# Performance work log

Hardware: AMD Instinct MI355X
Metric: run time of the kernel (lower is better)

The kernel has to match this reference:

```python
import jax, jax.numpy as jnp
import numpy as np

N = 50000   # nodes
E = 800000  # edges (avg degree 16)
C = 128     # hidden_channels
G = 128     # graphs in batch
L0, L1 = 512, 256  # linear_hidden_channels
P = 2       # num_params (output per graph)


def setup_inputs() -> dict:
    key = jax.random.key(0)
    ks = iter(jax.random.split(key, 48))

    def w(shape):
        return jax.random.normal(next(ks), shape, jnp.float32) / np.float32(np.sqrt(shape[0]))

    inp = {}
    inp["x"] = jax.random.normal(next(ks), (N, 4), jnp.float32)
    inp["edge_index"] = jax.random.randint(next(ks), (2, E), 0, N, dtype=jnp.int32)
    inp["edge_attr"] = jax.random.normal(next(ks), (E, 3), jnp.float32)
    inp["batch"] = jnp.sort(jax.random.randint(next(ks), (N,), 0, G, dtype=jnp.int32))
    # TransformerConv params: layer 0 (in=4) and shared layer (in=C, applied twice
    # because `[GConv(...)]*(n-1)` reuses the same module object).
    for i, din in enumerate([4, C]):
        inp[f"Wq{i}"] = w((din, C)); inp[f"bq{i}"] = jnp.zeros((C,), jnp.float32)
        inp[f"Wk{i}"] = w((din, C)); inp[f"bk{i}"] = jnp.zeros((C,), jnp.float32)
        inp[f"Wv{i}"] = w((din, C)); inp[f"bv{i}"] = jnp.zeros((C,), jnp.float32)
        inp[f"We{i}"] = w((3, C))   # lin_edge has no bias
        inp[f"Ws{i}"] = w((din, C)); inp[f"bs{i}"] = jnp.zeros((C,), jnp.float32)
    inp["Wl0"] = w((C, L0));  inp["bl0"] = jnp.zeros((L0,), jnp.float32)
    inp["Wl1"] = w((L0, L1)); inp["bl1"] = jnp.zeros((L1,), jnp.float32)
    inp["Wl2"] = w((L1, P));  inp["bl2"] = jnp.zeros((P,), jnp.float32)
    return inp


def tconv(x, src, dst, e_attr, Wq, bq, Wk, bk, Wv, bv, We, Ws, bs):
    # TransformerConv (heads=1, edge_dim, root_weight=True, beta=False)
    n = x.shape[0]
    c = Wq.shape[1]
    q = x @ Wq + bq            # [N, C]
    k = x @ Wk + bk
    v = x @ Wv + bv
    e = e_attr @ We            # [E, C]
    kj = k[src] + e            # [E, C] key at source + edge emb
    vj = v[src] + e            # [E, C] value at source + edge emb
    logits = jnp.sum(q[dst] * kj, axis=-1) / jnp.sqrt(jnp.float32(c))  # [E]
    # softmax over incoming edges of each target node
    m = jax.ops.segment_max(logits, dst, num_segments=n)
    a = jnp.exp(logits - m[dst])
    denom = jax.ops.segment_sum(a, dst, num_segments=n)
    alpha = a / denom[dst]
    out = jax.ops.segment_sum(vj * alpha[:, None], dst, num_segments=n)
    return out + x @ Ws + bs   # root/skip connection


def reference(x, edge_index, edge_attr, batch,
              Wq0, bq0, Wk0, bk0, Wv0, bv0, We0, Ws0, bs0,
              Wq1, bq1, Wk1, bk1, Wv1, bv1, We1, Ws1, bs1,
              Wl0, bl0, Wl1, bl1, Wl2, bl2):
    src, dst = edge_index[0], edge_index[1]
    # layer 0
    h = tconv(x, src, dst, edge_attr, Wq0, bq0, Wk0, bk0, Wv0, bv0, We0, Ws0, bs0)
    h = jax.nn.leaky_relu(h, 0.01)  # dropout is identity in eval
    # layers 1..2 share weights (Python list-multiplication of modules)
    for _ in range(2):
        h = tconv(h, src, dst, edge_attr, Wq1, bq1, Wk1, bk1, Wv1, bv1, We1, Ws1, bs1)
        h = jax.nn.leaky_relu(h, 0.01)
    # global_add_pool
    g = jax.ops.segment_sum(h, batch, num_segments=G)  # [G, C]
    # MLP head
    g = jax.nn.relu(g @ Wl0 + bl0)
    g = jax.nn.relu(g @ Wl1 + bl1)
    g = g @ Wl2 + bl2                                  # [G, 2]
    return jnp.ravel(g)                                # [G*2]
```

## Files before the change

### kernel.cpp

```cpp
#include <hip/hip_runtime.h>
#include <math.h>

#define N_NODES 50000
#define N_EDGES 800000
#define CDIM    128
#define GDIM    128
#define L0DIM   512
#define L1DIM   256

typedef unsigned int uint;
typedef unsigned short ushort;
typedef __attribute__((ext_vector_type(8))) short short8;
typedef __attribute__((ext_vector_type(4))) float f32x4;

#define QSCALE 0.12751744f

__device__ inline ushort f2bf(float f) {
  uint u = __float_as_uint(f);
  uint r = (u + 0x7fffu + ((u >> 16) & 1u)) >> 16;
  return (ushort)r;
}
__device__ inline float bflo(uint u) { return __uint_as_float(u << 16); }
__device__ inline float bfhi(uint u) { return __uint_as_float(u & 0xffff0000u); }

__global__ void hist_kernel(const int* __restrict__ dst, int* counts, int E) {
  int e = blockIdx.x * 256 + threadIdx.x;
  if (e < E) atomicAdd(&counts[dst[e]], 1);
}

__global__ void scan_blocks(const int* __restrict__ counts, int* excl, int* bsums, int N) {
  __shared__ int s[1024];
  int tid = threadIdx.x;
  int i = blockIdx.x * 1024 + tid;
  int v = (i < N) ? counts[i] : 0;
  s[tid] = v;
  __syncthreads();
  for (int off = 1; off < 1024; off <<= 1) {
    int t = (tid >= off) ? s[tid - off] : 0;
    __syncthreads();
    s[tid] += t;
    __syncthreads();
  }
  if (i < N) excl[i] = s[tid] - v;
  if (tid == 1023) bsums[blockIdx.x] = s[1023];
}

__global__ void scan_sums(int* bsums, int nb) {
  int lane = threadIdx.x;
  int orig = (lane < nb) ? bsums[lane] : 0;
  int v = orig;
#pragma unroll
  for (int off = 1; off < 64; off <<= 1) {
    int t = __shfl_up(v, off);
    if (lane >= off) v += t;
  }
  if (lane < nb) bsums[lane] = v - orig;
}

__global__ void scan_add(const int* __restrict__ excl, const int* __restrict__ bsums,
                         int* indptr, int N, int E) {
  int i = blockIdx.x * 1024 + threadIdx.x;
  if (i < N) indptr[i] = excl[i] + bsums[blockIdx.x];
  if (i == 0) indptr[N] = E;
}

__global__ void scatter2_kernel(const int* __restrict__ dst, const int* __restrict__ src,
                                const float* __restrict__ attr,
                                const int* __restrict__ indptr,
                                int* cursor, int* csr_src, float4* csr_attr, int E) {
  int e = blockIdx.x * 256 + threadIdx.x;
  if (e < E) {
    int d = dst[e];
    int pos = atomicAdd(&cursor[d], 1);
    int i = indptr[d] + pos;
    csr_src[i] = src[e];
    csr_attr[i] = make_float4(attr[e * 3 + 0], attr[e * 3 + 1], attr[e * 3 + 2], 0.f);
  }
}

__global__ void l0_qkvs(const float* __restrict__ x,
                        const float* __restrict__ Wq, const float* __restrict__ bq,
                        const float* __restrict__ Wk, const float* __restrict__ bk,
                        const float* __restrict__ Wv, const float* __restrict__ bv,
                        const float* __restrict__ Ws, const float* __restrict__ bs,
                        ushort* __restrict__ q, ushort* __restrict__ kvb,
                        float* __restrict__ hs, int N) {
  __shared__ float W[4][4][128];
  __shared__ float B[4][128];
  int tid = threadIdx.x;
  for (int i = tid; i < 4 * 128; i += 256) {
    W[0][i >> 7][i & 127] = Wq[i];
    W[1][i >> 7][i & 127] = Wk[i];
    W[2][i >> 7][i & 127] = Wv[i];
    W[3][i >> 7][i & 127] = Ws[i];
  }
  for (int i = tid; i < 128; i += 256) {
    B[0][i] = bq[i]; B[1][i] = bk[i]; B[2][i] = bv[i]; B[3][i] = bs[i];
  }
  __syncthreads();
  int gid = blockIdx.x * 256 + tid;
  int n = gid >> 7, c = gid & 127;
  if (n >= N) return;
  float x0 = x[n * 4 + 0], x1 = x[n * 4 + 1], x2 = x[n * 4 + 2], x3 = x[n * 4 + 3];
  float qv = x0 * W[0][0][c] + x1 * W[0][1][c] + x2 * W[0][2][c] + x3 * W[0][3][c] + B[0][c];
  float kv = x0 * W[1][0][c] + x1 * W[1][1][c] + x2 * W[1][2][c] + x3 * W[1][3][c] + B[1][c];
  float vv = x0 * W[2][0][c] + x1 * W[2][1][c] + x2 * W[2][2][c] + x3 * W[2][3][c] + B[2][c];
  float sv = x0 * W[3][0][c] + x1 * W[3][1][c] + x2 * W[3][2][c] + x3 * W[3][3][c] + B[3][c];
  q[(size_t)n * 128 + c] = f2bf(qv * QSCALE);
  kvb[(size_t)n * 256 + c]       = f2bf(kv);
  kvb[(size_t)n * 256 + 128 + c] = f2bf(vv);
  hs[n * 128 + c] = sv;
}

__global__ void prep_w(const float* __restrict__ Wq, const float* __restrict__ Wk,
                       const float* __restrict__ Wv, const float* __restrict__ Ws,
                       ushort* __restrict__ wt) {
  int idx = blockIdx.x * 256 + threadIdx.x;
  int z = idx >> 14, rem = idx & 16383;
  int k_ = rem >> 7, c_ = rem & 127;
  const float* W = (z == 0) ? Wq : (z == 1) ? Wk : (z == 2) ? Wv : Ws;
  wt[z * 16384 + c_ * 128 + k_] = f2bf(W[k_ * 128 + c_]);
}

#define LDA 136
__global__ __launch_bounds__(256) void gemm_mfma(
    const float* __restrict__ H, const ushort* __restrict__ wtg,
    const float* __restrict__ bq, const float* __restrict__ bk,
    const float* __restrict__ bv, const float* __restrict__ bs,
    ushort* __restrict__ q, ushort* __restrict__ kvb,
    float* __restrict__ hs, int N) {
  __shared__ ushort Alds[64 * LDA];
  __shared__ ushort Wlds[128 * LDA];
  int tid = threadIdx.x;
  int n0 = blockIdx.x * 64;

  {
    uint* al = (uint*)Alds;
    for (int i = tid; i < 4096; i += 256) {
      int r = i >> 6, kp = i & 63;
      int grow = n0 + r; grow = (grow < N) ? grow : (N - 1);
      float2 hv = *(const float2*)&H[(size_t)grow * 128 + 2 * kp];
      al[r * (LDA / 2) + kp] = (uint)f2bf(hv.x) | ((uint)f2bf(hv.y) << 16);
    }
  }

  int w = tid >> 6, lane = tid & 63;
  int m_ = lane & 15, quad = lane >> 4;

  for (int z = 0; z < 4; z++) {
    __syncthreads();
    {
      const uint* wg = (const uint*)(wtg + z * 16384);
      uint* wl = (uint*)Wlds;
      for (int i = tid; i < 8192; i += 256) {
        int c_ = i >> 6, kp = i & 63;
        wl[c_ * (LDA / 2) + kp] = wg[c_ * 64 + kp];
      }
    }
    __syncthreads();

    f32x4 acc[8];
#pragma unroll
    for (int ct = 0; ct < 8; ct++) acc[ct] = 0.f;

#pragma unroll
    for (int kc = 0; kc < 4; kc++) {
      short8 af = *(const short8*)&Alds[(w * 16 + m_) * LDA + kc * 32 + quad * 8];
#pragma unroll
      for (int ct = 0; ct < 8; ct++) {
        short8 bf = *(const short8*)&Wlds[(ct * 16 + m_) * LDA + kc * 32 + quad * 8];
        acc[ct] = __builtin_amdgcn_mfma_f32_16x16x32_bf16(af, bf, acc[ct], 0, 0, 0);
      }
    }

    const float* bb = (z == 0) ? bq : (z == 1) ? bk : (z == 2) ? bv : bs;
#pragma unroll
    for (int ct = 0; ct < 8; ct++) {
      int col = ct * 16 + m_;
      float bcol = bb[col];
#pragma unroll
      for (int reg = 0; reg < 4; reg++) {
        int n = n0 + w * 16 + quad * 4 + reg;
        if (n < N) {
          float o = acc[ct][reg] + bcol;
          if (z == 0)      q[(size_t)n * 128 + col] = f2bf(o * QSCALE);
          else if (z == 3) hs[(size_t)n * 128 + col] = o;
          else             kvb[(size_t)n * 256 + ((z == 2) ? 128 : 0) + col] = f2bf(o);
        }
      }
    }
  }
}

__global__ __launch_bounds__(256) void attn_fused(
    const ushort* __restrict__ q, const ushort* __restrict__ kv,
    const int* __restrict__ indptr, const int* __restrict__ csr_src,
    const float4* __restrict__ csr_attr, const float* __restrict__ We,
    float* __restrict__ h, int N) {
  __shared__ float WeS[384];
  int tid = threadIdx.x;
  for (int i = tid; i < 384; i += 256) WeS[i] = We[i];
  __syncthreads();
  int lane = tid & 63;
  int n = blockIdx.x * 4 + (tid >> 6);
  if (n >= N) return;
  int g = lane >> 4, gl = lane & 15;
  int c = gl * 8;
  uint4 qr = *(const uint4*)&q[(size_t)n * 128 + c];
  float qv[8] = {bflo(qr.x), bfhi(qr.x), bflo(qr.y), bfhi(qr.y),
                 bflo(qr.z), bfhi(qr.z), bflo(qr.w), bfhi(qr.w)};
  float we0[8], we1[8], we2[8];
#pragma unroll
  for (int j = 0; j < 8; j++) {
    we0[j] = WeS[c + j]; we1[j] = WeS[128 + c + j]; we2[j] = WeS[256 + c + j];
  }
  float t0 = 0.f, t1 = 0.f, t2 = 0.f;
#pragma unroll
  for (int j = 0; j < 8; j++) {
    t0 = fmaf(we0[j], qv[j], t0);
    t1 = fmaf(we1[j], qv[j], t1);
    t2 = fmaf(we2[j], qv[j], t2);
  }
#pragma unroll
  for (int off = 1; off < 16; off <<= 1) {
    t0 += __shfl_xor(t0, off);
    t1 += __shfl_xor(t1, off);
    t2 += __shfl_xor(t2, off);
  }

  float4 sk0 = *(const float4*)&h[(size_t)n * 128 + c];
  float4 sk1 = *(const float4*)&h[(size_t)n * 128 + c + 4];
  int beg = indptr[n], end = indptr[n + 1];

  if (end > beg) {
    float d = 0.f;
    float sa0 = 0.f, sa1 = 0.f, sa2 = 0.f;
    float acc[8];
#pragma unroll
    for (int j = 0; j < 8; j++) acc[j] = 0.f;
    const uint* kvw = (const uint*)kv;
    const int endm1 = end - 1;

    int i = beg + g;
    int pA = (i     < end) ? i     : endm1;
    int pB = (i + 4 < end) ? i + 4 : endm1;
    int sjA = csr_src[pA];  float4 atA = csr_attr[pA];
    int sjB = csr_src[pB];  float4 atB = csr_attr[pB];

    for (; i < end; i += 8) {
      int sjAc = sjA, sjBc = sjB;
      float4 atAc = atA, atBc = atB;
      float wB = ((i + 4) < end) ? 1.f : 0.f;
      int nn = i + 8;
      int qA = (nn     < end) ? nn     : endm1;
      int qB = (nn + 4 < end) ? nn + 4 : endm1;
      sjA = csr_src[qA]; atA = csr_attr[qA];
      sjB = csr_src[qB]; atB = csr_attr[qB];
      const uint4* kpA = (const uint4*)(kvw + (size_t)sjAc * 128);
      const uint4* kpB = (const uint4*)(kvw + (size_t)sjBc * 128);
      uint4 krA = kpA[gl];
      uint4 krB = kpB[gl];
      uint4 vrA = kpA[16 + gl];
      uint4 vrB = kpB[16 + gl];
      float kxA[8], kxB[8];
      kxA[0] = bflo(krA.x); kxA[1] = bfhi(krA.x); kxA[2] = bflo(krA.y); kxA[3] = bfhi(krA.y);
      kxA[4] = bflo(krA.z); kxA[5] = bfhi(krA.z); kxA[6] = bflo(krA.w); kxA[7] = bfhi(krA.w);
      kxB[0] = bflo(krB.x); kxB[1] = bfhi(krB.x); kxB[2] = bflo(krB.y); kxB[3] = bfhi(krB.y);
      kxB[4] = bflo(krB.z); kxB[5] = bfhi(krB.z); kxB[6] = bflo(krB.w); kxB[7] = bfhi(krB.w);
      float pAv = 0.f, pBv = 0.f;
#pragma unroll
      for (int j = 0; j < 8; j++) {
        pAv = fmaf(qv[j], kxA[j], pAv);
        pBv = fmaf(qv[j], kxB[j], pBv);
      }
      pAv += __shfl_xor(pAv, 1);  pBv += __shfl_xor(pBv, 1);
      pAv += __shfl_xor(pAv, 2);  pBv += __shfl_xor(pBv, 2);
      pAv += __shfl_xor(pAv, 4);  pBv += __shfl_xor(pBv, 4);
      pAv += __shfl_xor(pAv, 8);  pBv += __shfl_xor(pBv, 8);
      pAv = fmaf(atAc.x, t0, pAv);
      pBv = fmaf(atBc.x, t0, pBv);
      pAv = fmaf(atAc.y, t1, pAv);
      pBv = fmaf(atBc.y, t1, pBv);
      pAv = fmaf(atAc.z, t2, pAv);
      pBv = fmaf(atBc.z, t2, pBv);
      float aA = __builtin_amdgcn_exp2f(pAv);
      float aB = wB * __builtin_amdgcn_exp2f(pBv);
      d += aA + aB;
      sa0 = fmaf(aA, atAc.x, sa0); sa0 = fmaf(aB, atBc.x, sa0);
      sa1 = fmaf(aA, atAc.y, sa1); sa1 = fmaf(aB, atBc.y, sa1);
      sa2 = fmaf(aA, atAc.z, sa2); sa2 = fmaf(aB, atBc.z, sa2);
      float vxA[8], vxB[8];
      vxA[0] = bflo(vrA.x); vxA[1] = bfhi(vrA.x); vxA[2] = bflo(vrA.y); vxA[3] = bfhi(vrA.y);
      vxA[4] = bflo(vrA.z); vxA[5] = bfhi(vrA.z); vxA[6] = bflo(vrA.w); vxA[7] = bfhi(vrA.w);
      vxB[0] = bflo(vrB.x); vxB[1] = bfhi(vrB.x); vxB[2] = bflo(vrB.y); vxB[3] = bfhi(vrB.y);
      vxB[4] = bflo(vrB.z); vxB[5] = bfhi(vrB.z); vxB[6] = bflo(vrB.w); vxB[7] = bfhi(vrB.w);
#pragma unroll
      for (int j = 0; j < 8; j++) {
        acc[j] = fmaf(aA, vxA[j], acc[j]);
        acc[j] = fmaf(aB, vxB[j], acc[j]);
      }
    }
#pragma unroll
    for (int off = 16; off < 64; off <<= 1) {
      d += __shfl_xor(d, off);
      sa0 += __shfl_xor(sa0, off);
      sa1 += __shfl_xor(sa1, off);
      sa2 += __shfl_xor(sa2, off);
#pragma unroll
      for (int j = 0; j < 8; j++) acc[j] += __shfl_xor(acc[j], off);
    }
    float inv = 1.f / d;
    float o[8];
#pragma unroll
    for (int j = 0; j < 8; j++) {
      float ecorr = sa0 * we0[j] + sa1 * we1[j] + sa2 * we2[j];
      o[j] = (acc[j] + ecorr) * inv;
    }
    sk0.x += o[0]; sk0.y += o[1]; sk0.z += o[2]; sk0.w += o[3];
    sk1.x += o[4]; sk1.y += o[5]; sk1.z += o[6]; sk1.w += o[7];
  }
  sk0.x = (sk0.x > 0.f) ? sk0.x : 0.01f * sk0.x;
  sk0.y = (sk0.y > 0.f) ? sk0.y : 0.01f * sk0.y;
  sk0.z = (sk0.z > 0.f) ? sk0.z : 0.01f * sk0.z;
  sk0.w = (sk0.w > 0.f) ? sk0.w : 0.01f * sk0.w;
  sk1.x = (sk1.x > 0.f) ? sk1.x : 0.01f * sk1.x;
  sk1.y = (sk1.y > 0.f) ? sk1.y : 0.01f * sk1.y;
  sk1.z = (sk1.z > 0.f) ? sk1.z : 0.01f * sk1.z;
  sk1.w = (sk1.w > 0.f) ? sk1.w : 0.01f * sk1.w;
  if (g == 0) {
    *(float4*)&h[(size_t)n * 128 + c] = sk0;
    *(float4*)&h[(size_t)n * 128 + c + 4] = sk1;
  }
}

__global__ void pool_kernel(const float* __restrict__ h, const int* __restrict__ batch,
                            float* __restrict__ gout, int N) {
  int tid = threadIdx.x;
  int sub = tid >> 6;
  int c = 2 * (tid & 63);
  int n0 = blockIdx.x * 64 + sub * 16;
  if (n0 >= N) return;
  int n1 = min(n0 + 16, N);
  float a0 = 0.f, a1 = 0.f;
  int cur = batch[n0];
  for (int n = n0; n < n1; n++) {
    int b = batch[n];
    if (b != cur) {
      atomicAdd(&gout[cur * 128 + c], a0);
      atomicAdd(&gout[cur * 128 + c + 1], a1);
      a0 = 0.f; a1 = 0.f; cur = b;
    }
    float2 hv = *(const float2*)&h[(size_t)n * 128 + c];
    a0 += hv.x; a1 += hv.y;
  }
  atomicAdd(&gout[cur * 128 + c], a0);
  atomicAdd(&gout[cur * 128 + c + 1], a1);
}

__global__ __launch_bounds__(256) void mlp_fused(
    const float* __restrict__ gp,
    const float* __restrict__ Wl0, const float* __restrict__ bl0,
    const float* __restrict__ Wl1, const float* __restrict__ bl1,
    const float* __restrict__ Wl2, const float* __restrict__ bl2,
    float* __restrict__ out) {
  int g = blockIdx.x;
  int tid = threadIdx.x;
  __shared__ float xin[CDIM];
  __shared__ float h1[L0DIM];
  __shared__ float h2[L1DIM];
  __shared__ float r0s[4], r1s[4];
  if (tid < CDIM) xin[tid] = gp[g * CDIM + tid];
  __syncthreads();
  for (int c = tid; c < L0DIM; c += 256) {
    float a0 = 0.f, a1 = 0.f, a2 = 0.f, a3 = 0.f;
#pragma unroll 4
    for (int kk = 0; kk < CDIM; kk += 4) {
      a0 = fmaf(xin[kk + 0], Wl0[(kk + 0) * L0DIM + c], a0);
      a1 = fmaf(xin[kk + 1], Wl0[(kk + 1) * L0DIM + c], a1);
      a2 = fmaf(xin[kk + 2], Wl0[(kk + 2) * L0DIM + c], a2);
      a3 = fmaf(xin[kk + 3], Wl0[(kk + 3) * L0DIM + c], a3);
    }
    h1[c] = fmaxf((a0 + a1) + (a2 + a3) + bl0[c], 0.f);
  }
  __syncthreads();
  {
    int c = tid;
    float a0 = 0.f, a1 = 0.f, a2 = 0.f, a3 = 0.f;
#pragma unroll 4
    for (int kk = 0; kk < L0DIM; kk += 4) {
      a0 = fmaf(h1[kk + 0], Wl1[(kk + 0) * L1DIM + c], a0);
      a1 = fmaf(h1[kk + 1], Wl1[(kk + 1) * L1DIM + c], a1);
      a2 = fmaf(h1[kk + 2], Wl1[(kk + 2) * L1DIM + c], a2);
      a3 = fmaf(h1[kk + 3], Wl1[(kk + 3) * L1DIM + c], a3);
    }
    h2[c] = fmaxf((a0 + a1) + (a2 + a3) + bl1[c], 0.f);
  }
  __syncthreads();
  float p0 = h2[tid] * Wl2[tid * 2 + 0];
  float p1 = h2[tid] * Wl2[tid * 2 + 1];
#pragma unroll
  for (int off = 32; off > 0; off >>= 1) {
    p0 += __shfl_down(p0, off);
    p1 += __shfl_down(p1, off);
  }
  int wv = tid >> 6, ln = tid & 63;
  if (ln == 0) { r0s[wv] = p0; r1s[wv] = p1; }
  __syncthreads();
  if (tid == 0) out[g * 2 + 0] = r0s[0] + r0s[1] + r0s[2] + r0s[3] + bl2[0];
  if (tid == 1) out[g * 2 + 1] = r1s[0] + r1s[1] + r1s[2] + r1s[3] + bl2[1];
}

extern "C" void kernel_launch(void* const* d_in, const int* in_sizes, int n_in,
                              void* d_out, int out_size, void* d_ws, size_t ws_size,
                              hipStream_t stream) {
  const int N = N_NODES, E = N_EDGES;
  const float* x    = (const float*)d_in[0];
  const int*   ei   = (const int*)d_in[1];
  const float* attr = (const float*)d_in[2];
  const int*   batch= (const int*)d_in[3];
  const int* src = ei;
  const int* dst = ei + E;

  const float *Wq0 = (const float*)d_in[4],  *bq0 = (const float*)d_in[5];
  const float *Wk0 = (const float*)d_in[6],  *bk0 = (const float*)d_in[7];
  const float *Wv0 = (const float*)d_in[8],  *bv0 = (const float*)d_in[9];
  const float *We0 = (const float*)d_in[10];
  const float *Ws0 = (const float*)d_in[11], *bs0 = (const float*)d_in[12];
  const float *Wq1 = (const float*)d_in[13], *bq1 = (const float*)d_in[14];
  const float *Wk1 = (const float*)d_in[15], *bk1 = (const float*)d_in[16];
  const float *Wv1 = (const float*)d_in[17], *bv1 = (const float*)d_in[18];
  const float *We1 = (const float*)d_in[19];
  const float *Ws1 = (const float*)d_in[20], *bs1 = (const float*)d_in[21];
  const float *Wl0 = (const float*)d_in[22], *bl0 = (const float*)d_in[23];
  const float *Wl1 = (const float*)d_in[24], *bl1 = (const float*)d_in[25];
  const float *Wl2 = (const float*)d_in[26], *bl2 = (const float*)d_in[27];

  size_t off = 0;
  auto carve = [&](size_t bytes) {
    void* p = (char*)d_ws + off;
    off += (bytes + 255) & ~(size_t)255;
    return p;
  };
  float*  hA       = (float*)carve((size_t)N * CDIM * 4);
  float*  hB       = (float*)carve((size_t)N * CDIM * 4);
  ushort* qb       = (ushort*)carve((size_t)N * CDIM * 2);
  ushort* kvb      = (ushort*)carve((size_t)N * 256 * 2);
  int*    indptr   = (int*)carve((size_t)(N + 1) * 4);
  int*    csr_src  = (int*)carve((size_t)E * 4);
  float4* csr_attr = (float4*)carve((size_t)E * 16);
  int*    cc       = (int*)carve((size_t)2 * N * 4);
  int*    counts   = cc;
  int*    cursor   = cc + N;
  int*    excl     = (int*)carve((size_t)N * 4);
  int*    bsums    = (int*)carve((size_t)64 * 4);
  ushort* wt1      = (ushort*)carve((size_t)4 * 16384 * 2);
  float*  gp       = (float*)carve((size_t)GDIM * CDIM * 4);

  hipMemsetAsync(cc, 0, (size_t)2 * N * 4, stream);
  hipMemsetAsync(gp, 0, (size_t)GDIM * CDIM * 4, stream);

  int nscan = (N + 1023) / 1024;
  hist_kernel<<<(E + 255) / 256, 256, 0, stream>>>(dst, counts, E);
  scan_blocks<<<nscan, 1024, 0, stream>>>(counts, excl, bsums, N);
  scan_sums<<<1, 64, 0, stream>>>(bsums, nscan);
  scan_add<<<nscan, 1024, 0, stream>>>(excl, bsums, indptr, N, E);
  scatter2_kernel<<<(E + 255) / 256, 256, 0, stream>>>(dst, src, attr, indptr, cursor,
                                                       csr_src, csr_attr, E);
  prep_w<<<256, 256, 0, stream>>>(Wq1, Wk1, Wv1, Ws1, wt1);

  int naBlocks = (N + 3) / 4;
  int gemmBlocks = (N + 63) / 64;

  l0_qkvs<<<(N * 128 + 255) / 256, 256, 0, stream>>>(
      x, Wq0, bq0, Wk0, bk0, Wv0, bv0, Ws0, bs0, qb, kvb, hA, N);
  attn_fused<<<naBlocks, 256, 0, stream>>>(qb, kvb, indptr, csr_src, csr_attr, We0, hA, N);

  gemm_mfma<<<gemmBlocks, 256, 0, stream>>>(hA, wt1, bq1, bk1, bv1, bs1, qb, kvb, hB, N);
  attn_fused<<<naBlocks, 256, 0, stream>>>(qb, kvb, indptr, csr_src, csr_attr, We1, hB, N);

  gemm_mfma<<<gemmBlocks, 256, 0, stream>>>(hB, wt1, bq1, bk1, bv1, bs1, qb, kvb, hA, N);
  attn_fused<<<naBlocks, 256, 0, stream>>>(qb, kvb, indptr, csr_src, csr_attr, We1, hA, N);

  pool_kernel<<<(N + 63) / 64, 256, 0, stream>>>(hA, batch, gp, N);
  mlp_fused<<<GDIM, 256, 0, stream>>>(gp, Wl0, bl0, Wl1, bl1, Wl2, bl2, (float*)d_out);
}
```

Before: 609.4 us.

## Emit bf16 copy of node features and split GEMM over weight matrices via grid z

The attention and layer-0 kernels now also write a bf16 copy of the node features, so the GEMM reads half the bytes and skips the fp32-to-bf16 conversion. The GEMM is launched with a z-dimension of 4, one block per weight matrix (q, k, v, skip), instead of looping over all four inside one block. This gives four times as many blocks and removes the per-matrix syncs, at the cost of reloading the A tile four times and writing an extra bf16 buffer.

```diff
diff --git a/kernel.cpp b/kernel.cpp
--- a/kernel.cpp
+++ b/kernel.cpp
@@ -22,6 +22,9 @@
 }
 __device__ inline float bflo(uint u) { return __uint_as_float(u << 16); }
 __device__ inline float bfhi(uint u) { return __uint_as_float(u & 0xffff0000u); }
+__device__ inline uint pack2bf(float a, float b) {
+  return (uint)f2bf(a) | ((uint)f2bf(b) << 16);
+}
 
 __global__ void hist_kernel(const int* __restrict__ dst, int* counts, int E) {
   int e = blockIdx.x * 256 + threadIdx.x;
@@ -84,7 +87,7 @@
                         const float* __restrict__ Wv, const float* __restrict__ bv,
                         const float* __restrict__ Ws, const float* __restrict__ bs,
                         ushort* __restrict__ q, ushort* __restrict__ kvb,
-                        float* __restrict__ hs, int N) {
+                        float* __restrict__ hs, ushort* __restrict__ hb16, int N) {
   __shared__ float W[4][4][128];
   __shared__ float B[4][128];
   int tid = threadIdx.x;
@@ -109,7 +112,8 @@
   q[(size_t)n * 128 + c] = f2bf(qv * QSCALE);
   kvb[(size_t)n * 256 + c]       = f2bf(kv);
   kvb[(size_t)n * 256 + 128 + c] = f2bf(vv);
-  hs[n * 128 + c] = sv;
+  hs[(size_t)n * 128 + c] = sv;
+  hb16[(size_t)n * 128 + c] = f2bf(sv);
 }
 
 __global__ void prep_w(const float* __restrict__ Wq, const float* __restrict__ Wk,
@@ -124,69 +128,65 @@
 
 #define LDA 136
 __global__ __launch_bounds__(256) void gemm_mfma(
-    const float* __restrict__ H, const ushort* __restrict__ wtg,
+    const ushort* __restrict__ H16, const ushort* __restrict__ wtg,
     const float* __restrict__ bq, const float* __restrict__ bk,
     const float* __restrict__ bv, const float* __restrict__ bs,
     ushort* __restrict__ q, ushort* __restrict__ kvb,
     float* __restrict__ hs, int N) {
+  int z = blockIdx.z;
+  const float* bb = (z == 0) ? bq : (z == 1) ? bk : (z == 2) ? bv : bs;
   __shared__ ushort Alds[64 * LDA];
   __shared__ ushort Wlds[128 * LDA];
   int tid = threadIdx.x;
   int n0 = blockIdx.x * 64;
 
   {
+    const uint* wg = (const uint*)(wtg + z * 16384);
+    uint* wl = (uint*)Wlds;
+    for (int i = tid; i < 8192; i += 256) {
+      int c_ = i >> 6, kp = i & 63;
+      wl[c_ * (LDA / 2) + kp] = wg[c_ * 64 + kp];
+    }
+  }
+  {
+    const uint* hg = (const uint*)H16;
     uint* al = (uint*)Alds;
     for (int i = tid; i < 4096; i += 256) {
       int r = i >> 6, kp = i & 63;
       int grow = n0 + r; grow = (grow < N) ? grow : (N - 1);
-      float2 hv = *(const float2*)&H[(size_t)grow * 128 + 2 * kp];
-      al[r * (LDA / 2) + kp] = (uint)f2bf(hv.x) | ((uint)f2bf(hv.y) << 16);
-    }
-  }
+      al[r * (LDA / 2) + kp] = hg[(size_t)grow * 64 + kp];
+    }
+  }
+  __syncthreads();
 
   int w = tid >> 6, lane = tid & 63;
   int m_ = lane & 15, quad = lane >> 4;
-
-  for (int z = 0; z < 4; z++) {
-    __syncthreads();
-    {
-      const uint* wg = (const uint*)(wtg + z * 16384);
-      uint* wl = (uint*)Wlds;
-      for (int i = tid; i < 8192; i += 256) {
-        int c_ = i >> 6, kp = i & 63;
-        wl[c_ * (LDA / 2) + kp] = wg[c_ * 64 + kp];
-      }
-    }
-    __syncthreads();
-
-    f32x4 acc[8];
-#pragma unroll
-    for (int ct = 0; ct < 8; ct++) acc[ct] = 0.f;
-
-#pragma unroll
-    for (int kc = 0; kc < 4; kc++) {
-      short8 af = *(const short8*)&Alds[(w * 16 + m_) * LDA + kc * 32 + quad * 8];
-#pragma unroll
-      for (int ct = 0; ct < 8; ct++) {
-        short8 bf = *(const short8*)&Wlds[(ct * 16 + m_) * LDA + kc * 32 + quad * 8];
-        acc[ct] = __builtin_amdgcn_mfma_f32_16x16x32_bf16(af, bf, acc[ct], 0, 0, 0);
-      }
-    }
-
-    const float* bb = (z == 0) ? bq : (z == 1) ? bk : (z == 2) ? bv : bs;
+  f32x4 acc[8];
+#pragma unroll
+  for (int ct = 0; ct < 8; ct++) acc[ct] = 0.f;
+
+#pragma unroll
+  for (int kc = 0; kc < 4; kc++) {
+    short8 af = *(const short8*)&Alds[(w * 16 + m_) * LDA + kc * 32 + quad * 8];
 #pragma unroll
     for (int ct = 0; ct < 8; ct++) {
-      int col = ct * 16 + m_;
-      float bcol = bb[col];
-#pragma unroll
-      for (int reg = 0; reg < 4; reg++) {
-        int n = n0 + w * 16 + quad * 4 + reg;
-        if (n < N) {
-          float o = acc[ct][reg] + bcol;
-          if (z == 0)      q[(size_t)n * 128 + col] = f2bf(o * QSCALE);
-          else if (z == 3) hs[(size_t)n * 128 + col] = o;
-          else             kvb[(size_t)n * 256 + ((z == 2) ? 128 : 0) + col] = f2bf(o);
-        }
+      short8 bf = *(const short8*)&Wlds[(ct * 16 + m_) * LDA + kc * 32 + quad * 8];
+      acc[ct] = __builtin_amdgcn_mfma_f32_16x16x32_bf16(af, bf, acc[ct], 0, 0, 0);
+    }
+  }
+
+#pragma unroll
+  for (int ct = 0; ct < 8; ct++) {
+    int col = ct * 16 + m_;
+    float bcol = bb[col];
+#pragma unroll
+    for (int reg = 0; reg < 4; reg++) {
+      int n = n0 + w * 16 + quad * 4 + reg;
+      if (n < N) {
+        float o = acc[ct][reg] + bcol;
+        if (z == 0)      q[(size_t)n * 128 + col] = f2bf(o * QSCALE);
+        else if (z == 3) hs[(size_t)n * 128 + col] = o;
+        else             kvb[(size_t)n * 256 + ((z == 2) ? 128 : 0) + col] = f2bf(o);
       }
     }
   }
@@ -196,7 +196,7 @@
     const ushort* __restrict__ q, const ushort* __restrict__ kv,
     const int* __restrict__ indptr, const int* __restrict__ csr_src,
     const float4* __restrict__ csr_attr, const float* __restrict__ We,
-    float* __restrict__ h, int N) {
+    float* __restrict__ h, ushort* __restrict__ hb16, int N) {
   __shared__ float WeS[384];
   int tid = threadIdx.x;
   for (int i = tid; i < 384; i += 256) WeS[i] = We[i];
@@ -330,6 +330,12 @@
   if (g == 0) {
     *(float4*)&h[(size_t)n * 128 + c] = sk0;
     *(float4*)&h[(size_t)n * 128 + c + 4] = sk1;
+    uint4 hb;
+    hb.x = pack2bf(sk0.x, sk0.y);
+    hb.y = pack2bf(sk0.z, sk0.w);
+    hb.z = pack2bf(sk1.x, sk1.y);
+    hb.w = pack2bf(sk1.z, sk1.w);
+    *(uint4*)&hb16[(size_t)n * 128 + c] = hb;
   }
 }
 
@@ -443,6 +449,8 @@
   };
   float*  hA       = (float*)carve((size_t)N * CDIM * 4);
   float*  hB       = (float*)carve((size_t)N * CDIM * 4);
+  ushort* hA16     = (ushort*)carve((size_t)N * CDIM * 2);
+  ushort* hB16     = (ushort*)carve((size_t)N * CDIM * 2);
   ushort* qb       = (ushort*)carve((size_t)N * CDIM * 2);
   ushort* kvb      = (ushort*)carve((size_t)N * 256 * 2);
   int*    indptr   = (int*)carve((size_t)(N + 1) * 4);
@@ -469,17 +477,20 @@
   prep_w<<<256, 256, 0, stream>>>(Wq1, Wk1, Wv1, Ws1, wt1);
 
   int naBlocks = (N + 3) / 4;
-  int gemmBlocks = (N + 63) / 64;
+  dim3 gemmGrid((N + 63) / 64, 1, 4);
 
   l0_qkvs<<<(N * 128 + 255) / 256, 256, 0, stream>>>(
-      x, Wq0, bq0, Wk0, bk0, Wv0, bv0, Ws0, bs0, qb, kvb, hA, N);
-  attn_fused<<<naBlocks, 256, 0, stream>>>(qb, kvb, indptr, csr_src, csr_attr, We0, hA, N);
-
-  gemm_mfma<<<gemmBlocks, 256, 0, stream>>>(hA, wt1, bq1, bk1, bv1, bs1, qb, kvb, hB, N);
-  attn_fused<<<naBlocks, 256, 0, stream>>>(qb, kvb, indptr, csr_src, csr_attr, We1, hB, N);
-
-  gemm_mfma<<<gemmBlocks, 256, 0, stream>>>(hB, wt1, bq1, bk1, bv1, bs1, qb, kvb, hA, N);
-  attn_fused<<<naBlocks, 256, 0, stream>>>(qb, kvb, indptr, csr_src, csr_attr, We1, hA, N);
+      x, Wq0, bq0, Wk0, bk0, Wv0, bv0, Ws0, bs0, qb, kvb, hA, hA16, N);
+  attn_fused<<<naBlocks, 256, 0, stream>>>(qb, kvb, indptr, csr_src, csr_attr, We0,
+                                           hA, hA16, N);
+
+  gemm_mfma<<<gemmGrid, 256, 0, stream>>>(hA16, wt1, bq1, bk1, bv1, bs1, qb, kvb, hB, N);
+  attn_fused<<<naBlocks, 256, 0, stream>>>(qb, kvb, indptr, csr_src, csr_attr, We1,
+                                           hB, hB16, N);
+
+  gemm_mfma<<<gemmGrid, 256, 0, stream>>>(hB16, wt1, bq1, bk1, bv1, bs1, qb, kvb, hA, N);
+  attn_fused<<<naBlocks, 256, 0, stream>>>(qb, kvb, indptr, csr_src, csr_attr, We1,
+                                           hA, hA16, N);
 
   pool_kernel<<<(N + 63) / 64, 256, 0, stream>>>(hA, batch, gp, N);
   mlp_fused<<<GDIM, 256, 0, stream>>>(gp, Wl0, bl0, Wl1, bl1, Wl2, bl2, (float*)d_out);
```

Result: faster. 580.6 us (-4.7%).
